# Kernel tuning notes

Hardware: AMD Instinct MI355X
Metric: run time of the kernel (lower is better)

The kernel has to match this reference:

```python
import jax, jax.numpy as jnp
import numpy as np

B, N, H, D, E = 32, 1000, 256, 128, 512000
NB = B * N


def setup_inputs() -> dict:
    key = jax.random.key(0)
    ks = jax.random.split(key, 16)
    s = 0.05
    inp = {
        "x": jax.random.normal(ks[0], (B, D), jnp.float32),
        "h_prev": jax.random.normal(ks[1], (B, N, H), jnp.float32),
        "c_prev": jax.random.normal(ks[2], (B, N, H), jnp.float32),
        "src": jax.random.randint(ks[3], (E,), 0, NB, jnp.int32),
        "dst": jax.random.randint(ks[4], (E,), 0, NB, jnp.int32),
        "Wi": jax.random.normal(ks[5], (D, H), jnp.float32) * s,
        "bi": jax.random.normal(ks[6], (H,), jnp.float32) * s,
        "Wf": jax.random.normal(ks[7], (D, H), jnp.float32) * s,
        "bf": jax.random.normal(ks[8], (H,), jnp.float32) * s,
        "Wo": jax.random.normal(ks[9], (D, H), jnp.float32) * s,
        "bo": jax.random.normal(ks[10], (H,), jnp.float32) * s,
        "Wc": jax.random.normal(ks[11], (D, H), jnp.float32) * s,
        "bc": jax.random.normal(ks[12], (H,), jnp.float32) * s,
        "Wg": jax.random.normal(ks[13], (H, H), jnp.float32) * s,
        "bg": jax.random.normal(ks[14], (H,), jnp.float32) * s,
    }
    return inp


def _graph_conv(src, dst, h, Wg, bg):
    # DGL GraphConv, norm='both': D_dst^{-1/2} * sum_edges (D_src^{-1/2} * h_src) @ W + b
    nb = h.shape[0]
    ones = jnp.ones(src.shape[0], h.dtype)
    deg_out = jnp.maximum(jax.ops.segment_sum(ones, src, num_segments=nb), 1.0)
    deg_in = jnp.maximum(jax.ops.segment_sum(ones, dst, num_segments=nb), 1.0)
    h = h * (deg_out ** -0.5)[:, None]          # pre-normalize by src out-degree
    agg = jax.ops.segment_sum(h[src], dst, num_segments=nb)  # irregular gather/scatter
    agg = agg * (deg_in ** -0.5)[:, None]       # post-normalize by dst in-degree
    return agg @ Wg + bg


def reference(x, h_prev, c_prev, src, dst, Wi, bi, Wf, bf, Wo, bo, Wc, bc, Wg, bg):
    b, n, hh = h_prev.shape
    h_conv = _graph_conv(src, dst, h_prev.reshape(b * n, hh), Wg, bg).reshape(b, n, hh)
    # four input-gate projections, broadcast over nodes
    xi = (x @ Wi + bi)[:, None, :]
    xf = (x @ Wf + bf)[:, None, :]
    xo = (x @ Wo + bo)[:, None, :]
    xc = (x @ Wc + bc)[:, None, :]
    i_t = jax.nn.sigmoid(xi + h_conv)
    f_t = jax.nn.sigmoid(xf + h_conv)
    o_t = jax.nn.sigmoid(xo + h_conv)
    c_tilde = jnp.tanh(xc + h_conv)
    c_t = f_t * c_prev + i_t * c_tilde
    h_t = o_t * jnp.tanh(c_t)
    return h_t, c_t
```

## Files before the change

kernel.cpp:

```cpp
#include <hip/hip_runtime.h>

#define BB 32
#define NN 1000
#define HH 256
#define DD 128
#define EE 512000
#define NB (BB * NN)
#define NBKT 250
#define BKTCAP 2560
#define EPB 2000
#define NP1 256
#define PADS 64

#define GCURD_OFF 0
#define GCURS_OFF (NBKT)
#define DEGI_OFF 512
#define DEGO_OFF (512 + NB)
#define GATE_OFF (512 + 2 * NB)
#define WGB_OFF (GATE_OFF + 4 * BB * HH)
#define DSTB_OFF (WGB_OFF + (HH * HH) / 2)
#define SRCB_OFF (DSTB_OFF + NBKT * BKTCAP)
#define PAD_OFF (SRCB_OFF + NBKT * BKTCAP / 2)
#define HW_OFF (PAD_OFF + NB * PADS / 2)

using bf16x8 = __attribute__((ext_vector_type(8))) short;
using f32x4 = __attribute__((ext_vector_type(4))) float;

__device__ inline unsigned short f2bf(float x) {
    unsigned u = __float_as_uint(x);
    return (unsigned short)((u + 0x7FFFu + ((u >> 16) & 1u)) >> 16);
}
__device__ inline float bf2f(unsigned short u) {
    return __uint_as_float(((unsigned)u) << 16);
}

__global__ __launch_bounds__(256) void k_pre(
    const int* __restrict__ src, const int* __restrict__ dst,
    int* __restrict__ gcurD, int* __restrict__ gcurS,
    unsigned* __restrict__ dstb, unsigned short* __restrict__ srcb,
    const float* __restrict__ Wg, unsigned short* __restrict__ wgb,
    const float* __restrict__ x, const float* __restrict__ Wi,
    const float* __restrict__ bi, const float* __restrict__ Wf,
    const float* __restrict__ bf_, const float* __restrict__ Wo,
    const float* __restrict__ bo, const float* __restrict__ Wc,
    const float* __restrict__ bc, float* __restrict__ gates) {
    int blk = blockIdx.x;
    int t = threadIdx.x;
    if (blk < BB) {
        __shared__ float xs[DD];
        int b = blk;
        if (t < DD) xs[t] = x[b * DD + t];
        __syncthreads();
        float ai = bi[t], af = bf_[t], ao = bo[t], ac = bc[t];
#pragma unroll 4
        for (int k = 0; k < DD; k++) {
            float xv = xs[k];
            ai += xv * Wi[k * HH + t];
            af += xv * Wf[k * HH + t];
            ao += xv * Wo[k * HH + t];
            ac += xv * Wc[k * HH + t];
        }
        gates[0 * BB * HH + b * HH + t] = ai;
        gates[1 * BB * HH + b * HH + t] = af;
        gates[2 * BB * HH + b * HH + t] = ao;
        gates[3 * BB * HH + b * HH + t] = ac;
    } else if (blk < BB + 256) {
        int o = (blk - BB) * 256 + t;
        int j = o & 7;
        int c = o >> 3;
        int lane = c & 63;
        int nt = (c >> 6) & 15;
        int kk = c >> 10;
        int k = kk * 32 + (lane >> 4) * 8 + j;
        int n = nt * 16 + (lane & 15);
        wgb[o] = f2bf(Wg[k * HH + n]);
    } else {
        __shared__ int cntD[NBKT], cntS[NBKT], posD[NBKT], posS[NBKT];
        int pb = blk - (BB + 256);
        int e0 = pb * EPB;
        for (int i = t; i < NBKT; i += 256) {
            cntD[i] = 0;
            cntS[i] = 0;
        }
        __syncthreads();
        for (int i = t; i < EPB; i += 256) {
            int s = src[e0 + i];
            int d = dst[e0 + i];
            atomicAdd(&cntS[s >> 7], 1);
            atomicAdd(&cntD[d >> 7], 1);
        }
        __syncthreads();
        for (int i = t; i < NBKT; i += 256) {
            posD[i] = atomicAdd(&gcurD[i], cntD[i]);
            posS[i] = atomicAdd(&gcurS[i], cntS[i]);
        }
        __syncthreads();
        for (int i = t; i < EPB; i += 256) {
            int s = src[e0 + i];
            int d = dst[e0 + i];
            int bd = d >> 7, bs = s >> 7;
            int pd = atomicAdd(&posD[bd], 1);
            int ps = atomicAdd(&posS[bs], 1);
            dstb[bd * BKTCAP + pd] = ((unsigned)s << 16) | (unsigned)d;
            srcb[bs * BKTCAP + ps] = (unsigned short)s;
        }
    }
}

__global__ __launch_bounds__(256) void k_mid(
    const int* __restrict__ gcurD, const int* __restrict__ gcurS,
    const unsigned* __restrict__ dstb, const unsigned short* __restrict__ srcb,
    unsigned short* __restrict__ pad16, int* __restrict__ deg_in,
    int* __restrict__ deg_out, const float* __restrict__ h,
    const unsigned short* __restrict__ wgb, unsigned short* __restrict__ hw) {
    int blk = blockIdx.x;
    int t = threadIdx.x;
    if (blk < NB / 64) {
        int lane = t & 63;
        int w = t >> 6;
        int quad = lane >> 4;
        int mrow = lane & 15;
        int r0 = blk * 64 + w * 16;
        int row = r0 + mrow;

        f32x4 acc[16];
#pragma unroll
        for (int nt = 0; nt < 16; nt++) acc[nt] = (f32x4){0.f, 0.f, 0.f, 0.f};

#pragma unroll 1
        for (int kk = 0; kk < 8; kk++) {
            const float* ap = h + (size_t)row * HH + kk * 32 + quad * 8;
            float4 a0 = *(const float4*)ap;
            float4 a1 = *(const float4*)(ap + 4);
            bf16x8 af;
            af[0] = (short)f2bf(a0.x);
            af[1] = (short)f2bf(a0.y);
            af[2] = (short)f2bf(a0.z);
            af[3] = (short)f2bf(a0.w);
            af[4] = (short)f2bf(a1.x);
            af[5] = (short)f2bf(a1.y);
            af[6] = (short)f2bf(a1.z);
            af[7] = (short)f2bf(a1.w);
#pragma unroll
            for (int nt = 0; nt < 16; nt++) {
                bf16x8 bfr =
                    *(const bf16x8*)(wgb + (((kk * 16 + nt) * 64 + lane) << 3));
                acc[nt] = __builtin_amdgcn_mfma_f32_16x16x32_bf16(af, bfr,
                                                                  acc[nt], 0,
                                                                  0, 0);
            }
        }
#pragma unroll
        for (int nt = 0; nt < 16; nt++) {
#pragma unroll
            for (int reg = 0; reg < 4; reg++) {
                hw[(size_t)(r0 + quad * 4 + reg) * HH + nt * 16 + mrow] =
                    f2bf(acc[nt][reg]);
            }
        }
    } else if (blk < NB / 64 + NBKT) {
        __shared__ unsigned short lpad[128 * PADS];
        __shared__ int lcnt[128];
        int qb = blk - NB / 64;
        if (t < 128) lcnt[t] = 0;
        __syncthreads();
        int n = gcurD[qb];
        const unsigned* eb = dstb + qb * BKTCAP;
        for (int i = t; i < n; i += 256) {
            unsigned p = eb[i];
            int s = (int)(p >> 16);
            int dl = (int)(p & 127u);
            int q = atomicAdd(&lcnt[dl], 1);
            if (q < PADS) lpad[dl * PADS + q] = (unsigned short)s;
        }
        __syncthreads();
        int* gp = (int*)(pad16 + (size_t)qb * 128 * PADS);
        const int* lp = (const int*)lpad;
        for (int i = t; i < 128 * PADS / 2; i += 256) gp[i] = lp[i];
        if (t < 128) deg_in[qb * 128 + t] = lcnt[t];
    } else {
        __shared__ int scnt[128];
        int qb = blk - (NB / 64 + NBKT);
        if (t < 128) scnt[t] = 0;
        __syncthreads();
        int n = gcurS[qb];
        const unsigned short* sb = srcb + qb * BKTCAP;
        for (int i = t; i < n; i += 256) atomicAdd(&scnt[sb[i] & 127], 1);
        __syncthreads();
        if (t < 128) deg_out[qb * 128 + t] = scnt[t];
    }
}

__device__ inline void lstm1(float hc, float gi, float gf, float go, float gc,
                             float cp, float& ho, float& co) {
    float pi = gi + hc, pf = gf + hc, po = go + hc, pc = gc + hc;
    float it = 1.f / (1.f + __expf(-pi));
    float ft = 1.f / (1.f + __expf(-pf));
    float ot = 1.f / (1.f + __expf(-po));
    float e2 = __expf(2.f * pc);
    float ctl = (e2 - 1.f) / (e2 + 1.f);
    float ct = ft * cp + it * ctl;
    float e2c = __expf(2.f * ct);
    ho = ot * (e2c - 1.f) / (e2c + 1.f);
    co = ct;
}

__global__ __launch_bounds__(256) void k_out(
    const unsigned short* __restrict__ hw,
    const unsigned short* __restrict__ pad16, const int* __restrict__ deg_in,
    const int* __restrict__ deg_out, const float* __restrict__ bg,
    const float* __restrict__ gates, const float* __restrict__ c_prev,
    float* __restrict__ h_out, float* __restrict__ c_out) {
    int t = threadIdx.x;
    int lane = t & 63;
    int w = t >> 6;
    int node = blockIdx.x * 4 + w;
    int dcnt = deg_in[node];
    float si = rsqrtf((float)max(dcnt, 1));
    int cnt = min(dcnt, PADS);
    const unsigned short* pl = pad16 + (size_t)node * PADS;
    int col = lane * 4;
    const unsigned short* hwc = hw + col;

    float ax = 0.f, ay = 0.f, az = 0.f, aw = 0.f;
    int e = 0;
    for (; e + 8 <= cnt; e += 8) {
        ushort4 sa = *(const ushort4*)(pl + e);
        ushort4 sb = *(const ushort4*)(pl + e + 4);
        int s0 = sa.x, s1 = sa.y, s2 = sa.z, s3 = sa.w;
        int s4 = sb.x, s5 = sb.y, s6 = sb.z, s7 = sb.w;
        float c0 = rsqrtf((float)max(deg_out[s0], 1));
        float c1 = rsqrtf((float)max(deg_out[s1], 1));
        float c2 = rsqrtf((float)max(deg_out[s2], 1));
        float c3 = rsqrtf((float)max(deg_out[s3], 1));
        float c4 = rsqrtf((float)max(deg_out[s4], 1));
        float c5 = rsqrtf((float)max(deg_out[s5], 1));
        float c6 = rsqrtf((float)max(deg_out[s6], 1));
        float c7 = rsqrtf((float)max(deg_out[s7], 1));
        ushort4 q0 = *(const ushort4*)(hwc + ((size_t)s0 << 8));
        ushort4 q1 = *(const ushort4*)(hwc + ((size_t)s1 << 8));
        ushort4 q2 = *(const ushort4*)(hwc + ((size_t)s2 << 8));
        ushort4 q3 = *(const ushort4*)(hwc + ((size_t)s3 << 8));
        ushort4 q4 = *(const ushort4*)(hwc + ((size_t)s4 << 8));
        ushort4 q5 = *(const ushort4*)(hwc + ((size_t)s5 << 8));
        ushort4 q6 = *(const ushort4*)(hwc + ((size_t)s6 << 8));
        ushort4 q7 = *(const ushort4*)(hwc + ((size_t)s7 << 8));
        ax += ((c0 * bf2f(q0.x) + c1 * bf2f(q1.x)) +
               (c2 * bf2f(q2.x) + c3 * bf2f(q3.x))) +
              ((c4 * bf2f(q4.x) + c5 * bf2f(q5.x)) +
               (c6 * bf2f(q6.x) + c7 * bf2f(q7.x)));
        ay += ((c0 * bf2f(q0.y) + c1 * bf2f(q1.y)) +
               (c2 * bf2f(q2.y) + c3 * bf2f(q3.y))) +
              ((c4 * bf2f(q4.y) + c5 * bf2f(q5.y)) +
               (c6 * bf2f(q6.y) + c7 * bf2f(q7.y)));
        az += ((c0 * bf2f(q0.z) + c1 * bf2f(q1.z)) +
               (c2 * bf2f(q2.z) + c3 * bf2f(q3.z))) +
              ((c4 * bf2f(q4.z) + c5 * bf2f(q5.z)) +
               (c6 * bf2f(q6.z) + c7 * bf2f(q7.z)));
        aw += ((c0 * bf2f(q0.w) + c1 * bf2f(q1.w)) +
               (c2 * bf2f(q2.w) + c3 * bf2f(q3.w))) +
              ((c4 * bf2f(q4.w) + c5 * bf2f(q5.w)) +
               (c6 * bf2f(q6.w) + c7 * bf2f(q7.w)));
    }
    for (; e < cnt; e++) {
        int s = pl[e];
        float cc = rsqrtf((float)max(deg_out[s], 1));
        ushort4 q = *(const ushort4*)(hwc + ((size_t)s << 8));
        ax += cc * bf2f(q.x);
        ay += cc * bf2f(q.y);
        az += cc * bf2f(q.z);
        aw += cc * bf2f(q.w);
    }

    int b = node / NN;
    float4 bgv = *(const float4*)(bg + col);
    float4 gi = *(const float4*)(gates + 0 * BB * HH + b * HH + col);
    float4 gf = *(const float4*)(gates + 1 * BB * HH + b * HH + col);
    float4 go = *(const float4*)(gates + 2 * BB * HH + b * HH + col);
    float4 gc = *(const float4*)(gates + 3 * BB * HH + b * HH + col);
    float4 cp = *(const float4*)(c_prev + (size_t)node * HH + col);

    float4 ho, co;
    lstm1(ax * si + bgv.x, gi.x, gf.x, go.x, gc.x, cp.x, ho.x, co.x);
    lstm1(ay * si + bgv.y, gi.y, gf.y, go.y, gc.y, cp.y, ho.y, co.y);
    lstm1(az * si + bgv.z, gi.z, gf.z, go.z, gc.z, cp.z, ho.z, co.z);
    lstm1(aw * si + bgv.w, gi.w, gf.w, go.w, gc.w, cp.w, ho.w, co.w);

    *(float4*)(h_out + (size_t)node * HH + col) = ho;
    *(float4*)(c_out + (size_t)node * HH + col) = co;
}

extern "C" void kernel_launch(void* const* d_in, const int* in_sizes, int n_in,
                              void* d_out, int out_size, void* d_ws,
                              size_t ws_size, hipStream_t stream) {
    const float* x = (const float*)d_in[0];
    const float* h_prev = (const float*)d_in[1];
    const float* c_prev = (const float*)d_in[2];
    const int* src = (const int*)d_in[3];
    const int* dst = (const int*)d_in[4];
    const float* Wi = (const float*)d_in[5];
    const float* bi = (const float*)d_in[6];
    const float* Wf = (const float*)d_in[7];
    const float* bf_ = (const float*)d_in[8];
    const float* Wo = (const float*)d_in[9];
    const float* bo = (const float*)d_in[10];
    const float* Wc = (const float*)d_in[11];
    const float* bc = (const float*)d_in[12];
    const float* Wg = (const float*)d_in[13];
    const float* bg = (const float*)d_in[14];

    int* wsi = (int*)d_ws;
    float* wsf = (float*)d_ws;
    int* gcurD = wsi + GCURD_OFF;
    int* gcurS = wsi + GCURS_OFF;
    int* deg_in = wsi + DEGI_OFF;
    int* deg_out = wsi + DEGO_OFF;
    float* gates = wsf + GATE_OFF;
    unsigned short* wgb = (unsigned short*)(wsi + WGB_OFF);
    unsigned* dstb = (unsigned*)(wsi + DSTB_OFF);
    unsigned short* srcb = (unsigned short*)(wsi + SRCB_OFF);
    unsigned short* pad16 = (unsigned short*)(wsi + PAD_OFF);
    unsigned short* hw = (unsigned short*)(wsi + HW_OFF);
    float* h_out = (float*)d_out;
    float* c_out = h_out + (size_t)NB * HH;

    hipMemsetAsync(gcurD, 0, (size_t)2 * NBKT * 4, stream);

    k_pre<<<BB + 256 + NP1, 256, 0, stream>>>(src, dst, gcurD, gcurS, dstb,
                                              srcb, Wg, wgb, x, Wi, bi, Wf,
                                              bf_, Wo, bo, Wc, bc, gates);
    k_mid<<<NB / 64 + 2 * NBKT, 256, 0, stream>>>(gcurD, gcurS, dstb, srcb,
                                                  pad16, deg_in, deg_out,
                                                  h_prev, wgb, hw);
    k_out<<<NB / 4, 256, 0, stream>>>(hw, pad16, deg_in, deg_out, bg, gates,
                                      c_prev, h_out, c_out);
}
```

Measured before the change: 238.1 us.

## Overlap edge bucketing with MFMA projection and precompute degree rsqrt

Restructures the kernel schedule. Edge bucketing now runs in the same launch as the h@Wg MFMA GEMM so the two overlap, and the hipMemset is replaced by zeroing inside the prep kernel. The per-bucket CSR/degree pass becomes its own kernel that stores rsqrt of the in- and out-degrees as floats, so k_out loads ready coefficients instead of recomputing rsqrt per gathered edge. This adds one kernel launch in exchange for the overlap and the cheaper gather loop.

```diff
diff --git a/kernel.cpp b/kernel.cpp
--- a/kernel.cpp
+++ b/kernel.cpp
@@ -15,8 +15,9 @@
 #define GCURD_OFF 0
 #define GCURS_OFF (NBKT)
 #define DEGI_OFF 512
-#define DEGO_OFF (512 + NB)
-#define GATE_OFF (512 + 2 * NB)
+#define DSOF_OFF (512 + NB)
+#define DSIF_OFF (512 + 2 * NB)
+#define GATE_OFF (512 + 3 * NB)
 #define WGB_OFF (GATE_OFF + 4 * BB * HH)
 #define DSTB_OFF (WGB_OFF + (HH * HH) / 2)
 #define SRCB_OFF (DSTB_OFF + NBKT * BKTCAP)
@@ -34,21 +35,29 @@
     return __uint_as_float(((unsigned)u) << 16);
 }
 
-__global__ __launch_bounds__(256) void k_pre(
-    const int* __restrict__ src, const int* __restrict__ dst,
-    int* __restrict__ gcurD, int* __restrict__ gcurS,
-    unsigned* __restrict__ dstb, unsigned short* __restrict__ srcb,
+__global__ __launch_bounds__(256) void k_prep(
     const float* __restrict__ Wg, unsigned short* __restrict__ wgb,
-    const float* __restrict__ x, const float* __restrict__ Wi,
-    const float* __restrict__ bi, const float* __restrict__ Wf,
-    const float* __restrict__ bf_, const float* __restrict__ Wo,
-    const float* __restrict__ bo, const float* __restrict__ Wc,
-    const float* __restrict__ bc, float* __restrict__ gates) {
+    int* __restrict__ gcur, const float* __restrict__ x,
+    const float* __restrict__ Wi, const float* __restrict__ bi,
+    const float* __restrict__ Wf, const float* __restrict__ bf_,
+    const float* __restrict__ Wo, const float* __restrict__ bo,
+    const float* __restrict__ Wc, const float* __restrict__ bc,
+    float* __restrict__ gates) {
     int blk = blockIdx.x;
     int t = threadIdx.x;
-    if (blk < BB) {
+    if (blk < 256) {
+        int o = blk * 256 + t;
+        int j = o & 7;
+        int c = o >> 3;
+        int lane = c & 63;
+        int nt = (c >> 6) & 15;
+        int kk = c >> 10;
+        int k = kk * 32 + (lane >> 4) * 8 + j;
+        int n = nt * 16 + (lane & 15);
+        wgb[o] = f2bf(Wg[k * HH + n]);
+    } else if (blk < 256 + BB) {
         __shared__ float xs[DD];
-        int b = blk;
+        int b = blk - 256;
         if (t < DD) xs[t] = x[b * DD + t];
         __syncthreads();
         float ai = bi[t], af = bf_[t], ao = bo[t], ac = bc[t];
@@ -64,55 +73,18 @@
         gates[1 * BB * HH + b * HH + t] = af;
         gates[2 * BB * HH + b * HH + t] = ao;
         gates[3 * BB * HH + b * HH + t] = ac;
-    } else if (blk < BB + 256) {
-        int o = (blk - BB) * 256 + t;
-        int j = o & 7;
-        int c = o >> 3;
-        int lane = c & 63;
-        int nt = (c >> 6) & 15;
-        int kk = c >> 10;
-        int k = kk * 32 + (lane >> 4) * 8 + j;
-        int n = nt * 16 + (lane & 15);
-        wgb[o] = f2bf(Wg[k * HH + n]);
     } else {
-        __shared__ int cntD[NBKT], cntS[NBKT], posD[NBKT], posS[NBKT];
-        int pb = blk - (BB + 256);
-        int e0 = pb * EPB;
-        for (int i = t; i < NBKT; i += 256) {
-            cntD[i] = 0;
-            cntS[i] = 0;
-        }
-        __syncthreads();
-        for (int i = t; i < EPB; i += 256) {
-            int s = src[e0 + i];
-            int d = dst[e0 + i];
-            atomicAdd(&cntS[s >> 7], 1);
-            atomicAdd(&cntD[d >> 7], 1);
-        }
-        __syncthreads();
-        for (int i = t; i < NBKT; i += 256) {
-            posD[i] = atomicAdd(&gcurD[i], cntD[i]);
-            posS[i] = atomicAdd(&gcurS[i], cntS[i]);
-        }
-        __syncthreads();
-        for (int i = t; i < EPB; i += 256) {
-            int s = src[e0 + i];
-            int d = dst[e0 + i];
-            int bd = d >> 7, bs = s >> 7;
-            int pd = atomicAdd(&posD[bd], 1);
-            int ps = atomicAdd(&posS[bs], 1);
-            dstb[bd * BKTCAP + pd] = ((unsigned)s << 16) | (unsigned)d;
-            srcb[bs * BKTCAP + ps] = (unsigned short)s;
-        }
-    }
-}
-
-__global__ __launch_bounds__(256) void k_mid(
-    const int* __restrict__ gcurD, const int* __restrict__ gcurS,
-    const unsigned* __restrict__ dstb, const unsigned short* __restrict__ srcb,
-    unsigned short* __restrict__ pad16, int* __restrict__ deg_in,
-    int* __restrict__ deg_out, const float* __restrict__ h,
-    const unsigned short* __restrict__ wgb, unsigned short* __restrict__ hw) {
+        gcur[t] = 0;
+        gcur[256 + t] = 0;
+    }
+}
+
+__global__ __launch_bounds__(256) void k_main(
+    const int* __restrict__ src, const int* __restrict__ dst,
+    int* __restrict__ gcurD, int* __restrict__ gcurS,
+    unsigned* __restrict__ dstb, unsigned short* __restrict__ srcb,
+    const float* __restrict__ h, const unsigned short* __restrict__ wgb,
+    unsigned short* __restrict__ hw) {
     int blk = blockIdx.x;
     int t = threadIdx.x;
     if (blk < NB / 64) {
@@ -158,10 +130,50 @@
                     f2bf(acc[nt][reg]);
             }
         }
-    } else if (blk < NB / 64 + NBKT) {
+    } else {
+        __shared__ int cntD[NBKT], cntS[NBKT], posD[NBKT], posS[NBKT];
+        int pb = blk - NB / 64;
+        int e0 = pb * EPB;
+        for (int i = t; i < NBKT; i += 256) {
+            cntD[i] = 0;
+            cntS[i] = 0;
+        }
+        __syncthreads();
+        for (int i = t; i < EPB; i += 256) {
+            int s = src[e0 + i];
+            int d = dst[e0 + i];
+            atomicAdd(&cntS[s >> 7], 1);
+            atomicAdd(&cntD[d >> 7], 1);
+        }
+        __syncthreads();
+        for (int i = t; i < NBKT; i += 256) {
+            posD[i] = atomicAdd(&gcurD[i], cntD[i]);
+            posS[i] = atomicAdd(&gcurS[i], cntS[i]);
+        }
+        __syncthreads();
+        for (int i = t; i < EPB; i += 256) {
+            int s = src[e0 + i];
+            int d = dst[e0 + i];
+            int bd = d >> 7, bs = s >> 7;
+            int pd = atomicAdd(&posD[bd], 1);
+            int ps = atomicAdd(&posS[bs], 1);
+            dstb[bd * BKTCAP + pd] = ((unsigned)s << 16) | (unsigned)d;
+            srcb[bs * BKTCAP + ps] = (unsigned short)s;
+        }
+    }
+}
+
+__global__ __launch_bounds__(256) void k_csr(
+    const int* __restrict__ gcurD, const int* __restrict__ gcurS,
+    const unsigned* __restrict__ dstb, const unsigned short* __restrict__ srcb,
+    unsigned short* __restrict__ pad16, int* __restrict__ deg_in,
+    float* __restrict__ dsif, float* __restrict__ dsof) {
+    int blk = blockIdx.x;
+    int t = threadIdx.x;
+    if (blk < NBKT) {
         __shared__ unsigned short lpad[128 * PADS];
         __shared__ int lcnt[128];
-        int qb = blk - NB / 64;
+        int qb = blk;
         if (t < 128) lcnt[t] = 0;
         __syncthreads();
         int n = gcurD[qb];
@@ -177,17 +189,21 @@
         int* gp = (int*)(pad16 + (size_t)qb * 128 * PADS);
         const int* lp = (const int*)lpad;
         for (int i = t; i < 128 * PADS / 2; i += 256) gp[i] = lp[i];
-        if (t < 128) deg_in[qb * 128 + t] = lcnt[t];
+        if (t < 128) {
+            int c = lcnt[t];
+            deg_in[qb * 128 + t] = c;
+            dsif[qb * 128 + t] = rsqrtf((float)max(c, 1));
+        }
     } else {
         __shared__ int scnt[128];
-        int qb = blk - (NB / 64 + NBKT);
+        int qb = blk - NBKT;
         if (t < 128) scnt[t] = 0;
         __syncthreads();
         int n = gcurS[qb];
         const unsigned short* sb = srcb + qb * BKTCAP;
         for (int i = t; i < n; i += 256) atomicAdd(&scnt[sb[i] & 127], 1);
         __syncthreads();
-        if (t < 128) deg_out[qb * 128 + t] = scnt[t];
+        if (t < 128) dsof[qb * 128 + t] = rsqrtf((float)max(scnt[t], 1));
     }
 }
 
@@ -208,16 +224,16 @@
 __global__ __launch_bounds__(256) void k_out(
     const unsigned short* __restrict__ hw,
     const unsigned short* __restrict__ pad16, const int* __restrict__ deg_in,
-    const int* __restrict__ deg_out, const float* __restrict__ bg,
-    const float* __restrict__ gates, const float* __restrict__ c_prev,
-    float* __restrict__ h_out, float* __restrict__ c_out) {
+    const float* __restrict__ dsif, const float* __restrict__ dsof,
+    const float* __restrict__ bg, const float* __restrict__ gates,
+    const float* __restrict__ c_prev, float* __restrict__ h_out,
+    float* __restrict__ c_out) {
     int t = threadIdx.x;
     int lane = t & 63;
     int w = t >> 6;
     int node = blockIdx.x * 4 + w;
-    int dcnt = deg_in[node];
-    float si = rsqrtf((float)max(dcnt, 1));
-    int cnt = min(dcnt, PADS);
+    float si = dsif[node];
+    int cnt = min(deg_in[node], PADS);
     const unsigned short* pl = pad16 + (size_t)node * PADS;
     int col = lane * 4;
     const unsigned short* hwc = hw + col;
@@ -229,14 +245,14 @@
         ushort4 sb = *(const ushort4*)(pl + e + 4);
         int s0 = sa.x, s1 = sa.y, s2 = sa.z, s3 = sa.w;
         int s4 = sb.x, s5 = sb.y, s6 = sb.z, s7 = sb.w;
-        float c0 = rsqrtf((float)max(deg_out[s0], 1));
-        float c1 = rsqrtf((float)max(deg_out[s1], 1));
-        float c2 = rsqrtf((float)max(deg_out[s2], 1));
-        float c3 = rsqrtf((float)max(deg_out[s3], 1));
-        float c4 = rsqrtf((float)max(deg_out[s4], 1));
-        float c5 = rsqrtf((float)max(deg_out[s5], 1));
-        float c6 = rsqrtf((float)max(deg_out[s6], 1));
-        float c7 = rsqrtf((float)max(deg_out[s7], 1));
+        float c0 = dsof[s0];
+        float c1 = dsof[s1];
+        float c2 = dsof[s2];
+        float c3 = dsof[s3];
+        float c4 = dsof[s4];
+        float c5 = dsof[s5];
+        float c6 = dsof[s6];
+        float c7 = dsof[s7];
         ushort4 q0 = *(const ushort4*)(hwc + ((size_t)s0 << 8));
         ushort4 q1 = *(const ushort4*)(hwc + ((size_t)s1 << 8));
         ushort4 q2 = *(const ushort4*)(hwc + ((size_t)s2 << 8));
@@ -264,7 +280,7 @@
     }
     for (; e < cnt; e++) {
         int s = pl[e];
-        float cc = rsqrtf((float)max(deg_out[s], 1));
+        float cc = dsof[s];
         ushort4 q = *(const ushort4*)(hwc + ((size_t)s << 8));
         ax += cc * bf2f(q.x);
         ay += cc * bf2f(q.y);
@@ -314,7 +330,8 @@
     int* gcurD = wsi + GCURD_OFF;
     int* gcurS = wsi + GCURS_OFF;
     int* deg_in = wsi + DEGI_OFF;
-    int* deg_out = wsi + DEGO_OFF;
+    float* dsof = wsf + DSOF_OFF;
+    float* dsif = wsf + DSIF_OFF;
     float* gates = wsf + GATE_OFF;
     unsigned short* wgb = (unsigned short*)(wsi + WGB_OFF);
     unsigned* dstb = (unsigned*)(wsi + DSTB_OFF);
@@ -324,14 +341,12 @@
     float* h_out = (float*)d_out;
     float* c_out = h_out + (size_t)NB * HH;
 
-    hipMemsetAsync(gcurD, 0, (size_t)2 * NBKT * 4, stream);
-
-    k_pre<<<BB + 256 + NP1, 256, 0, stream>>>(src, dst, gcurD, gcurS, dstb,
-                                              srcb, Wg, wgb, x, Wi, bi, Wf,
-                                              bf_, Wo, bo, Wc, bc, gates);
-    k_mid<<<NB / 64 + 2 * NBKT, 256, 0, stream>>>(gcurD, gcurS, dstb, srcb,
-                                                  pad16, deg_in, deg_out,
-                                                  h_prev, wgb, hw);
-    k_out<<<NB / 4, 256, 0, stream>>>(hw, pad16, deg_in, deg_out, bg, gates,
-                                      c_prev, h_out, c_out);
-}
+    k_prep<<<256 + BB + 1, 256, 0, stream>>>(Wg, wgb, gcurD, x, Wi, bi, Wf,
+                                             bf_, Wo, bo, Wc, bc, gates);
+    k_main<<<NB / 64 + NP1, 256, 0, stream>>>(src, dst, gcurD, gcurS, dstb,
+                                              srcb, h_prev, wgb, hw);
+    k_csr<<<2 * NBKT, 256, 0, stream>>>(gcurD, gcurS, dstb, srcb, pad16,
+                                        deg_in, dsif, dsof);
+    k_out<<<NB / 4, 256, 0, stream>>>(hw, pad16, deg_in, dsif, dsof, bg,
+                                      gates, c_prev, h_out, c_out);
+}
```

Result: no change. 239.9 us (+0.8%).
